# Performance work log

Measured on AMD Instinct MI355X. Metric: run time of the kernel, lower is better.

## Reference

```python
import jax, jax.numpy as jnp
import numpy as np

VOCAB, D = 10000, 32
QUEUE_LEN = 100


def setup_inputs() -> dict:
    key = jax.random.key(0)
    ks = jax.random.split(key, 8)
    B, T = 64, 1024
    s = 0.1
    return dict(
        inputs=jax.random.randint(ks[0], (B, T), 0, 10000, dtype=jnp.int32),
        emb=jax.random.normal(ks[1], (VOCAB, D), dtype=jnp.float32) * s,
        k_lstm=jax.random.normal(ks[2], (D, 4 * D), dtype=jnp.float32) * s,
        rk_lstm=jax.random.normal(ks[3], (D, 4 * D), dtype=jnp.float32) * s,
        b_lstm=jnp.zeros((4 * D,), dtype=jnp.float32),
        W1=jax.random.normal(ks[4], (D, D), dtype=jnp.float32) * s,
        b1=jnp.zeros((D,), dtype=jnp.float32),
        W2=jax.random.normal(ks[5], (D, 1), dtype=jnp.float32) * s,
        b2=jnp.zeros((1,), dtype=jnp.float32),
    )


def _lstm(x, k, rk, b):
    # Keras LSTM, gate order [i, f, g(cell), o], sigmoid recurrent act, tanh act.
    B, T, D = x.shape
    xg = jnp.einsum('btd,de->bte', x, k) + b  # precompute input projections

    def step(carry, xg_t):
        h, c = carry
        z = xg_t + h @ rk
        i, f, g, o = jnp.split(z, 4, axis=-1)
        c = jax.nn.sigmoid(f) * c + jax.nn.sigmoid(i) * jnp.tanh(g)
        h = jax.nn.sigmoid(o) * jnp.tanh(c)
        return (h, c), h

    init = (jnp.zeros((B, D), x.dtype), jnp.zeros((B, D), x.dtype))
    _, hs = jax.lax.scan(step, init, jnp.swapaxes(xg, 0, 1))  # [T,B,D]
    return jnp.swapaxes(hs, 0, 1)  # [B,T,D]


def _zero_index_queue(x_ids):
    # Vectorized replacement of the (i,j) Python scan: last QUEUE_LEN positions
    # (row-major order) where token==0, as [QUEUE_LEN,2] int32, padded with -1.
    B, T = x_ids.shape
    flat = (x_ids == 0).reshape(-1)
    N = flat.shape[0]
    ridx = jnp.nonzero(flat[::-1], size=QUEUE_LEN, fill_value=-1)[0]
    pos = jnp.where(ridx >= 0, N - 1 - ridx, -1)[::-1]  # ascending, like deque
    ii = jnp.where(pos >= 0, pos // T, -1)
    jj = jnp.where(pos >= 0, pos % T, -1)
    return jnp.stack([ii, jj], axis=-1).astype(jnp.int32)


def _forward_float(x_ids, emb, k_lstm, rk_lstm, b_lstm, W1, b1, W2, b2):
    x = emb[x_ids]                                  # [B,T,D]
    h = _lstm(x, k_lstm, rk_lstm, b_lstm)           # [B,T,D]
    scores = jnp.einsum('btd,bsd->bts', h, h)       # unscaled dot attention
    attn = jax.nn.softmax(scores, axis=-1)
    ctx = jnp.einsum('bts,bsd->btd', attn, h)       # Keras Attention output
    y = jnp.einsum('btd,bte->bde', ctx, h)          # Dot(axes=(1,1)) -> [B,D,D]
    y = jax.nn.relu(y @ W1 + b1)
    return jax.nn.sigmoid(y @ W2 + b2)              # [B,D,1]


def reference(inputs, emb, k_lstm, rk_lstm, b_lstm, W1, b1, W2, b2):
    x_ids = jnp.where(inputs < VOCAB, inputs, 0)
    out = _forward_float(x_ids, emb, k_lstm, rk_lstm, b_lstm, W1, b1, W2, b2)
    return out, _zero_index_queue(x_ids)
```

## Files before the change

### kernel.cpp

```cpp
#include <hip/hip_runtime.h>
#include <math.h>

#define BB 64
#define TT 1024
#define DD 32
#define GG 128
#define VOCABN 10000
#define QLEN 100

typedef short short8 __attribute__((ext_vector_type(8)));
typedef float floatx4 __attribute__((ext_vector_type(4)));
typedef float floatx2 __attribute__((ext_vector_type(2)));
typedef unsigned short u16;

__device__ __forceinline__ float fsig(float x) {
    return __builtin_amdgcn_rcpf(1.0f + __expf(-x));
}
__device__ __forceinline__ float readlane_f(float v, int l) {
    return __int_as_float(__builtin_amdgcn_readlane(__float_as_int(v), l));
}
__device__ __forceinline__ u16 f2bf_rne(float x) {
    unsigned u = __float_as_uint(x);
    u += 0x7FFF + ((u >> 16) & 1);
    return (u16)(u >> 16);
}
__device__ __forceinline__ float bf2f(u16 s) {
    return __uint_as_float(((unsigned)s) << 16);
}
__device__ __forceinline__ floatx2 fma2(float s, floatx2 w, floatx2 acc) {
    return __builtin_elementwise_fma((floatx2){s, s}, w, acc);
}

#define UU 8
__global__
__attribute__((amdgpu_flat_work_group_size(128, 128)))
__attribute__((amdgpu_waves_per_eu(1, 1)))
void k_lstm_scan(const int* __restrict__ ids,
                 const float* __restrict__ emb,
                 const float* __restrict__ klstm,
                 const float* __restrict__ bias,
                 const float* __restrict__ rk,
                 u16* __restrict__ hh, u16* __restrict__ hl,
                 u16* __restrict__ th, u16* __restrict__ tl,
                 int* __restrict__ list,
                 float* __restrict__ outq) {
    const int b = blockIdx.x;
    const int tid = threadIdx.x;
    const int wv = tid >> 6;
    const int l = tid & 63;
    if (b >= BB) {
        if (wv != 0) return;
        const int4* v4 = (const int4*)ids;
        const int C4 = (BB * TT) / 4 / 64;
        const int b4 = l * C4;
        int cnt = 0;
#pragma unroll 4
        for (int i = 0; i < C4; ++i) {
            int4 v = v4[b4 + i];
            cnt += (v.x == 0 || (unsigned)v.x >= VOCABN);
            cnt += (v.y == 0 || (unsigned)v.y >= VOCABN);
            cnt += (v.z == 0 || (unsigned)v.z >= VOCABN);
            cnt += (v.w == 0 || (unsigned)v.w >= VOCABN);
        }
        int scan = cnt;
#pragma unroll
        for (int o = 1; o < 64; o <<= 1) {
            int nn = __shfl_up(scan, o);
            if (l >= o) scan += nn;
        }
        const int total = __shfl(scan, 63);
        int off = scan - cnt;
        const int base = l * (C4 * 4);
#pragma unroll 4
        for (int i = 0; i < C4; ++i) {
            int4 v = v4[b4 + i];
            if (v.x == 0 || (unsigned)v.x >= VOCABN) list[off++] = base + 4 * i;
            if (v.y == 0 || (unsigned)v.y >= VOCABN) list[off++] = base + 4 * i + 1;
            if (v.z == 0 || (unsigned)v.z >= VOCABN) list[off++] = base + 4 * i + 2;
            if (v.w == 0 || (unsigned)v.w >= VOCABN) list[off++] = base + 4 * i + 3;
        }
        __threadfence();
        const int Kc = total < QLEN ? total : QLEN;
        for (int t = l; t < QLEN; t += 64) {
            float ii = -1.0f, jj = -1.0f;
            if (t >= QLEN - Kc) {
                int pos = list[total - QLEN + t];
                ii = (float)(pos >> 10);
                jj = (float)(pos & (TT - 1));
            }
            outq[2 * t] = ii;
            outq[2 * t + 1] = jj;
        }
        return;
    }

    __shared__ float ring[2][UU][GG];
    __shared__ __align__(16) float hring[2][UU][DD];
    const int* idsb = ids + b * TT;

    if (wv == 1) {
        const int ja = l, jb = l + 64;
        floatx2 kp[DD];
#pragma unroll
        for (int d2 = 0; d2 < DD; ++d2)
            kp[d2] = (floatx2){klstm[d2 * GG + ja], klstm[d2 * GG + jb]};
        const floatx2 bj = (floatx2){bias[ja], bias[jb]};
        const int dd = l & 31;
        const int u_r = l >> 3, dc = (l & 7) * 4;
        const int d_c = l & 31, ug = (l >> 5) * 4;
        u16* hhb = hh + (size_t)b * TT * DD;
        u16* hlb = hl + (size_t)b * TT * DD;
        u16* thb = th + (size_t)b * DD * TT;
        u16* tlb = tl + (size_t)b * DD * TT;

#define PROD_TOKEN(SEL, U, EV)                                               \
        {                                                                    \
            floatx2 z0 = bj;                                                 \
            floatx2 z1 = {0.f, 0.f}, z2 = {0.f, 0.f}, z3 = {0.f, 0.f};       \
            _Pragma("unroll")                                                \
            for (int k = 0; k < DD; k += 4) {                                \
                float e0 = readlane_f(EV, k);                                \
                float e1 = readlane_f(EV, k + 1);                            \
                float e2 = readlane_f(EV, k + 2);                            \
                float e3 = readlane_f(EV, k + 3);                            \
                z0 = fma2(e0, kp[k], z0);                                    \
                z1 = fma2(e1, kp[k + 1], z1);                                \
                z2 = fma2(e2, kp[k + 2], z2);                                \
                z3 = fma2(e3, kp[k + 3], z3);                                \
            }                                                                \
            floatx2 zf = (z0 + z1) + (z2 + z3);                              \
            ring[SEL][U][ja] = zf.x;                                         \
            ring[SEL][U][jb] = zf.y;                                         \
        }

#define CVT_CHUNK(HSEL, TC0)                                                 \
        {                                                                    \
            const float4 hv4 = *(const float4*)&hring[HSEL][u_r][dc];        \
            float xr[4] = {hv4.x, hv4.y, hv4.z, hv4.w};                      \
            u16 rh[4], rl[4];                                                \
            _Pragma("unroll")                                                \
            for (int i = 0; i < 4; ++i) {                                    \
                rh[i] = f2bf_rne(xr[i]);                                     \
                rl[i] = f2bf_rne(xr[i] - bf2f(rh[i]));                       \
            }                                                                \
            ushort4 rhv = {rh[0], rh[1], rh[2], rh[3]};                      \
            ushort4 rlv = {rl[0], rl[1], rl[2], rl[3]};                      \
            *(ushort4*)&hhb[(size_t)((TC0) + u_r) * DD + dc] = rhv;          \
            *(ushort4*)&hlb[(size_t)((TC0) + u_r) * DD + dc] = rlv;          \
            u16 ch[4], cl[4];                                                \
            _Pragma("unroll")                                                \
            for (int j = 0; j < 4; ++j) {                                    \
                float x = hring[HSEL][ug + j][d_c];                          \
                ch[j] = f2bf_rne(x);                                         \
                cl[j] = f2bf_rne(x - bf2f(ch[j]));                           \
            }                                                                \
            ushort4 chv = {ch[0], ch[1], ch[2], ch[3]};                      \
            ushort4 clv = {cl[0], cl[1], cl[2], cl[3]};                      \
            *(ushort4*)&thb[(size_t)d_c * TT + (TC0) + ug] = chv;            \
            *(ushort4*)&tlb[(size_t)d_c * TT + (TC0) + ug] = clv;            \
        }

        {
            int id0 = idsb[0]; if ((unsigned)id0 >= VOCABN) id0 = 0;
            float ec = emb[id0 * DD + dd];
#pragma unroll
            for (int u = 0; u < UU; ++u) {
                float en = 0.f;
                if (u + 1 < UU) {
                    int idn = idsb[u + 1]; if ((unsigned)idn >= VOCABN) idn = 0;
                    en = emb[idn * DD + dd];
                }
                PROD_TOKEN(0, u, ec)
                ec = en;
            }
        }
        __syncthreads();
        int sel = 0;
        for (int t0 = 0; t0 < TT; t0 += UU) {
            if (t0 + UU < TT) {
                const int s = sel ^ 1;
                int id0 = idsb[t0 + UU]; if ((unsigned)id0 >= VOCABN) id0 = 0;
                float ec = emb[id0 * DD + dd];
#pragma unroll
                for (int u = 0; u < UU; ++u) {
                    float en = 0.f;
                    if (u + 1 < UU) {
                        int tn = t0 + UU + u + 1;
                        if (tn > TT - 1) tn = TT - 1;
                        int idn = idsb[tn]; if ((unsigned)idn >= VOCABN) idn = 0;
                        en = emb[idn * DD + dd];
                    }
                    PROD_TOKEN(s, u, ec)
                    ec = en;
                }
            }
            if (t0) CVT_CHUNK((t0 / UU - 1) & 1, t0 - UU)
            __syncthreads();
            sel ^= 1;
        }
        CVT_CHUNK(1, TT - UU)
#undef PROD_TOKEN
#undef CVT_CHUNK
        return;
    }

    const int d = l & 31;
    const bool hi = l >= 32;
    const int ga = (hi ? 32 : 0) + d;
    const int gb = (hi ? 96 : 64) + d;
    floatx2 rkp[DD];
#pragma unroll
    for (int k = 0; k < DD; ++k)
        rkp[k] = (floatx2){rk[k * GG + ga], rk[k * GG + gb]};

    float h = 0.0f, c = 0.0f;
    __syncthreads();
    int sel = 0;
    for (int t0 = 0; t0 < TT; t0 += UU) {
        float pa[UU], pb[UU];
#pragma unroll
        for (int u = 0; u < UU; ++u) {
            pa[u] = ring[sel][u][ga];
            pb[u] = ring[sel][u][gb];
        }
#pragma unroll
        for (int u = 0; u < UU; ++u) {
            floatx2 x0 = {pa[u], pb[u]};
            floatx2 x1 = {0.f, 0.f}, x2 = {0.f, 0.f}, x3 = {0.f, 0.f};
#pragma unroll
            for (int k = 0; k < DD; k += 4) {
                float h0 = readlane_f(h, k);
                float h1 = readlane_f(h, k + 1);
                float h2 = readlane_f(h, k + 2);
                float h3 = readlane_f(h, k + 3);
                x0 = fma2(h0, rkp[k],     x0);
                x1 = fma2(h1, rkp[k + 1], x1);
                x2 = fma2(h2, rkp[k + 2], x2);
                x3 = fma2(h3, rkp[k + 3], x3);
            }
            floatx2 zf = (x0 + x1) + (x2 + x3);
            float za = zf.x, zb = zf.y;
            float a = fsig(za);
            float zbm = hi ? zb : 2.0f * zb;
            float s2 = fsig(zbm);
            float bv = hi ? s2 : 2.0f * s2 - 1.0f;
            auto r1 = __builtin_amdgcn_permlane32_swap(
                __float_as_int(bv), __float_as_int(a), false, false);
            auto r2 = __builtin_amdgcn_permlane32_swap(
                __float_as_int(a), __float_as_int(bv), false, false);
            float fg = __int_as_float(r1[0]);
            float og = __int_as_float(r2[0]);
            c = fmaf(fg, c, a * bv);
            float tc = 2.0f * fsig(2.0f * c) - 1.0f;
            h = og * tc;
            if (!hi) hring[sel][u][d] = h;
        }
        __syncthreads();
        sel ^= 1;
    }
}

__global__ __launch_bounds__(256, 1) void k_attn(const u16* __restrict__ hh,
                                                 const u16* __restrict__ hl,
                                                 const u16* __restrict__ th,
                                                 const u16* __restrict__ tl,
                                                 u16* __restrict__ cth,
                                                 u16* __restrict__ ctl) {
    __shared__ __align__(16) char smem[4][20480];
    const int tid = threadIdx.x;
    const int w = tid >> 6;
    const int l = tid & 63;
    const int m = l & 15;
    const int g = l >> 4;
    const int b = blockIdx.x & 63;
    const int qt = (blockIdx.x >> 6) * 4 + w;
    const int q0 = qt * 64;
    const size_t rb = (size_t)b * TT * DD;
    const size_t tb = (size_t)b * DD * TT;
    u16* plw = (u16*)smem[w];

    const short8 Qh0 = *(const short8*)&hh[rb + (size_t)(q0 + m) * DD + g * 8];
    const short8 Ql0 = *(const short8*)&hl[rb + (size_t)(q0 + m) * DD + g * 8];
    const short8 Qh1 = *(const short8*)&hh[rb + (size_t)(q0 + 16 + m) * DD + g * 8];
    const short8 Ql1 = *(const short8*)&hl[rb + (size_t)(q0 + 16 + m) * DD + g * 8];
    const short8 Qh2 = *(const short8*)&hh[rb + (size_t)(q0 + 32 + m) * DD + g * 8];
    const short8 Ql2 = *(const short8*)&hl[rb + (size_t)(q0 + 32 + m) * DD + g * 8];
    const short8 Qh3 = *(const short8*)&hh[rb + (size_t)(q0 + 48 + m) * DD + g * 8];
    const short8 Ql3 = *(const short8*)&hl[rb + (size_t)(q0 + 48 + m) * DD + g * 8];
    short8 ONES;
#pragma unroll
    for (int j = 0; j < 8; ++j) ONES[j] = (short)0x3F80;

    floatx4 c0 = {0.f, 0.f, 0.f, 0.f}, c1 = {0.f, 0.f, 0.f, 0.f};
    floatx4 c2 = {0.f, 0.f, 0.f, 0.f}, c3 = {0.f, 0.f, 0.f, 0.f};
    floatx4 c4 = {0.f, 0.f, 0.f, 0.f}, c5 = {0.f, 0.f, 0.f, 0.f};
    floatx4 c6 = {0.f, 0.f, 0.f, 0.f}, c7 = {0.f, 0.f, 0.f, 0.f};
    floatx4 la0 = {0.f, 0.f, 0.f, 0.f}, la1 = {0.f, 0.f, 0.f, 0.f};
    floatx4 la2 = {0.f, 0.f, 0.f, 0.f}, la3 = {0.f, 0.f, 0.f, 0.f};

#define S_BLOCK(QH, QL, KH_A, KL_A, KH_B, KL_B, SA, SB)                       \
    SA = __builtin_amdgcn_mfma_f32_16x16x32_bf16(QH, KH_A, SA, 0, 0, 0);      \
    SA = __builtin_amdgcn_mfma_f32_16x16x32_bf16(QH, KL_A, SA, 0, 0, 0);      \
    SA = __builtin_amdgcn_mfma_f32_16x16x32_bf16(QL, KH_A, SA, 0, 0, 0);      \
    SB = __builtin_amdgcn_mfma_f32_16x16x32_bf16(QH, KH_B, SB, 0, 0, 0);      \
    SB = __builtin_amdgcn_mfma_f32_16x16x32_bf16(QH, KL_B, SB, 0, 0, 0);      \
    SB = __builtin_amdgcn_mfma_f32_16x16x32_bf16(QL, KH_B, SB, 0, 0, 0);

#define EXP_STORE(SA, SB, TILE, SLOT, PN)                                     \
    {                                                                         \
        u16* lp = plw + (((TILE) * 2 + (SLOT)) * 2 + (PN)) * 640;             \
        _Pragma("unroll")                                                     \
        for (int r = 0; r < 4; ++r) {                                         \
            lp[(g * 4 + r) * 40 + m]      = f2bf_rne(__expf(SA[r]));          \
            lp[(g * 4 + r) * 40 + 16 + m] = f2bf_rne(__expf(SB[r]));          \
        }                                                                     \
    }

#define SPANEL(KhA, KlA, KhB, KlB, SLOT, PN)                                  \
    {                                                                         \
        floatx4 sA = {0.f, 0.f, 0.f, 0.f}, sB = {0.f, 0.f, 0.f, 0.f};         \
        floatx4 tA = {0.f, 0.f, 0.f, 0.f}, tB = {0.f, 0.f, 0.f, 0.f};         \
        floatx4 uA = {0.f, 0.f, 0.f, 0.f}, uB = {0.f, 0.f, 0.f, 0.f};         \
        floatx4 vA = {0.f, 0.f, 0.f, 0.f}, vB = {0.f, 0.f, 0.f, 0.f};         \
        S_BLOCK(Qh0, Ql0, KhA, KlA, KhB, KlB, sA, sB)                         \
        S_BLOCK(Qh1, Ql1, KhA, KlA, KhB, KlB, tA, tB)                         \
        S_BLOCK(Qh2, Ql2, KhA, KlA, KhB, KlB, uA, uB)                         \
        S_BLOCK(Qh3, Ql3, KhA, KlA, KhB, KlB, vA, vB)                         \
        EXP_STORE(sA, sB, 0, SLOT, PN)                                        \
        EXP_STORE(tA, tB, 1, SLOT, PN)                                        \
        EXP_STORE(uA, uB, 2, SLOT, PN)                                        \
        EXP_STORE(vA, vB, 3, SLOT, PN)                                        \
    }

#define PV_TILE(T, CA, CB, LAc, SLOTP, PN, VH0, VL0, VH1, VL1)                \
    {                                                                         \
        const short8 P = *(const short8*)&plw[(((T) * 2 + (SLOTP)) * 2 + (PN)) * 640 + m * 40 + g * 8]; \
        CA  = __builtin_amdgcn_mfma_f32_16x16x32_bf16(P, VH0, CA, 0, 0, 0);   \
        CA  = __builtin_amdgcn_mfma_f32_16x16x32_bf16(P, VL0, CA, 0, 0, 0);   \
        CB  = __builtin_amdgcn_mfma_f32_16x16x32_bf16(P, VH1, CB, 0, 0, 0);   \
        CB  = __builtin_amdgcn_mfma_f32_16x16x32_bf16(P, VL1, CB, 0, 0, 0);   \
        LAc = __builtin_amdgcn_mfma_f32_16x16x32_bf16(P, ONES, LAc, 0, 0, 0); \
    }

#define PV_PANEL(SLOTP, PN, VH0, VL0, VH1, VL1)                               \
    PV_TILE(0, c0, c1, la0, SLOTP, PN, VH0, VL0, VH1, VL1)                    \
    PV_TILE(1, c2, c3, la1, SLOTP, PN, VH0, VL0, VH1, VL1)                    \
    PV_TILE(2, c4, c5, la2, SLOTP, PN, VH0, VL0, VH1, VL1)                    \
    PV_TILE(3, c6, c7, la3, SLOTP, PN, VH0, VL0, VH1, VL1)

#define LOAD_K(BASE, RA, RLA, RB, RLB)                                        \
    RA  = *(const short8*)&hh[rb + (size_t)((BASE) + m) * DD + g * 8];        \
    RLA = *(const short8*)&hl[rb + (size_t)((BASE) + m) * DD + g * 8];        \
    RB  = *(const short8*)&hh[rb + (size_t)((BASE) + 16 + m) * DD + g * 8];   \
    RLB = *(const short8*)&hl[rb + (size_t)((BASE) + 16 + m) * DD + g * 8];

#define LOAD_V(BASE, RH0, RL0, RH1, RL1)                                      \
    RH0 = *(const short8*)&th[tb + (size_t)m * TT + (BASE) + g * 8];          \
    RL0 = *(const short8*)&tl[tb + (size_t)m * TT + (BASE) + g * 8];          \
    RH1 = *(const short8*)&th[tb + (size_t)(16 + m) * TT + (BASE) + g * 8];   \
    RL1 = *(const short8*)&tl[tb + (size_t)(16 + m) * TT + (BASE) + g * 8];

    {
        short8 KA, KLA, KB, KLB;
        LOAD_K(0, KA, KLA, KB, KLB)
        SPANEL(KA, KLA, KB, KLB, 0, 0)
        LOAD_K(32, KA, KLA, KB, KLB)
        SPANEL(KA, KLA, KB, KLB, 0, 1)
    }
    short8 V0h0, V0l0, V0h1, V0l1, V1h0, V1l0, V1h1, V1l1;
    short8 K0hA, K0lA, K0hB, K0lB, K1hA, K1lA, K1hB, K1lB;
    LOAD_V(0,  V0h0, V0l0, V0h1, V0l1)
    LOAD_V(32, V1h0, V1l0, V1h1, V1l1)
    LOAD_K(64, K0hA, K0lA, K0hB, K0lB)
    LOAD_K(96, K1hA, K1lA, K1hB, K1lB)

#pragma unroll 1
    for (int j = 1; j < 16; ++j) {
        const int kb = (j < 15) ? 64 * (j + 1) : 0;
        const int vb = 64 * j;
        short8 nK0hA, nK0lA, nK0hB, nK0lB, nK1hA, nK1lA, nK1hB, nK1lB;
        short8 nV0h0, nV0l0, nV0h1, nV0l1, nV1h0, nV1l0, nV1h1, nV1l1;
        LOAD_K(kb,      nK0hA, nK0lA, nK0hB, nK0lB)
        LOAD_K(kb + 32, nK1hA, nK1lA, nK1hB, nK1lB)
        LOAD_V(vb,      nV0h0, nV0l0, nV0h1, nV0l1)
        LOAD_V(vb + 32, nV1h0, nV1l0, nV1h1, nV1l1)

        const int sl = j & 1;
        SPANEL(K0hA, K0lA, K0hB, K0lB, sl, 0)
        SPANEL(K1hA, K1lA, K1hB, K1lB, sl, 1)

        const int sp = (j - 1) & 1;
        PV_PANEL(sp, 0, V0h0, V0l0, V0h1, V0l1)
        PV_PANEL(sp, 1, V1h0, V1l0, V1h1, V1l1)

        K0hA = nK0hA; K0lA = nK0lA; K0hB = nK0hB; K0lB = nK0lB;
        K1hA = nK1hA; K1lA = nK1lA; K1hB = nK1hB; K1lB = nK1lB;
        V0h0 = nV0h0; V0l0 = nV0l0; V0h1 = nV0h1; V0l1 = nV0l1;
        V1h0 = nV1h0; V1l0 = nV1l0; V1h1 = nV1h1; V1l1 = nV1l1;
    }
    PV_PANEL(1, 0, V0h0, V0l0, V0h1, V0l1)
    PV_PANEL(1, 1, V1h0, V1l0, V1h1, V1l1)
#undef S_BLOCK
#undef EXP_STORE
#undef SPANEL
#undef PV_TILE
#undef PV_PANEL
#undef LOAD_K
#undef LOAD_V

    float (*ct)[34] = (float (*)[34])smem[w];
#pragma unroll
    for (int r = 0; r < 4; ++r) {
        float li0 = __builtin_amdgcn_rcpf(la0[r]);
        float li1 = __builtin_amdgcn_rcpf(la1[r]);
        float li2 = __builtin_amdgcn_rcpf(la2[r]);
        float li3 = __builtin_amdgcn_rcpf(la3[r]);
        ct[g * 4 + r][m]            = c0[r] * li0;
        ct[g * 4 + r][16 + m]       = c1[r] * li0;
        ct[16 + g * 4 + r][m]       = c2[r] * li1;
        ct[16 + g * 4 + r][16 + m]  = c3[r] * li1;
        ct[32 + g * 4 + r][m]       = c4[r] * li2;
        ct[32 + g * 4 + r][16 + m]  = c5[r] * li2;
        ct[48 + g * 4 + r][m]       = c6[r] * li3;
        ct[48 + g * 4 + r][16 + m]  = c7[r] * li3;
    }
    const int srow = l >> 3;
    const int tcol = (l & 7) * 8;
#pragma unroll
    for (int cblk = 0; cblk < 4; ++cblk) {
        const int dr = cblk * 8 + srow;
        short8 hvec, lvec;
#pragma unroll
        for (int j2 = 0; j2 < 8; ++j2) {
            float v = ct[tcol + j2][dr];
            u16 hv = f2bf_rne(v);
            hvec[j2] = (short)hv;
            lvec[j2] = (short)f2bf_rne(v - bf2f(hv));
        }
        *(short8*)&cth[tb + (size_t)dr * TT + q0 + tcol] = hvec;
        *(short8*)&ctl[tb + (size_t)dr * TT + q0 + tcol] = lvec;
    }
}

__global__ __launch_bounds__(256) void k_ymlp(const u16* __restrict__ cth,
                                              const u16* __restrict__ ctl,
                                              const u16* __restrict__ th,
                                              const u16* __restrict__ tl,
                                              const float* __restrict__ W1,
                                              const float* __restrict__ b1,
                                              const float* __restrict__ W2,
                                              const float* __restrict__ b2,
                                              float* __restrict__ out) {
    const int b = blockIdx.x;
    const int tid = threadIdx.x;
    const int w = tid >> 6;
    const int l = tid & 63;
    const int m = l & 15;
    const int g = l >> 4;
    const size_t tb = (size_t)b * DD * TT;
    const int k0 = w * (TT / 4);

    floatx4 y00 = {0.f, 0.f, 0.f, 0.f}, y01 = {0.f, 0.f, 0.f, 0.f};
    floatx4 y10 = {0.f, 0.f, 0.f, 0.f}, y11 = {0.f, 0.f, 0.f, 0.f};
#pragma unroll 2
    for (int ks = 0; ks < TT / 4; ks += 32) {
        const size_t kk = (size_t)(k0 + ks + g * 8);
        short8 A0h = *(const short8*)&cth[tb + (size_t)m * TT + kk];
        short8 A0l = *(const short8*)&ctl[tb + (size_t)m * TT + kk];
        short8 A1h = *(const short8*)&cth[tb + (size_t)(16 + m) * TT + kk];
        short8 A1l = *(const short8*)&ctl[tb + (size_t)(16 + m) * TT + kk];
        short8 B0h = *(const short8*)&th[tb + (size_t)m * TT + kk];
        short8 B0l = *(const short8*)&tl[tb + (size_t)m * TT + kk];
        short8 B1h = *(const short8*)&th[tb + (size_t)(16 + m) * TT + kk];
        short8 B1l = *(const short8*)&tl[tb + (size_t)(16 + m) * TT + kk];
        y00 = __builtin_amdgcn_mfma_f32_16x16x32_bf16(A0h, B0h, y00, 0, 0, 0);
        y00 = __builtin_amdgcn_mfma_f32_16x16x32_bf16(A0h, B0l, y00, 0, 0, 0);
        y00 = __builtin_amdgcn_mfma_f32_16x16x32_bf16(A0l, B0h, y00, 0, 0, 0);
        y01 = __builtin_amdgcn_mfma_f32_16x16x32_bf16(A0h, B1h, y01, 0, 0, 0);
        y01 = __builtin_amdgcn_mfma_f32_16x16x32_bf16(A0h, B1l, y01, 0, 0, 0);
        y01 = __builtin_amdgcn_mfma_f32_16x16x32_bf16(A0l, B1h, y01, 0, 0, 0);
        y10 = __builtin_amdgcn_mfma_f32_16x16x32_bf16(A1h, B0h, y10, 0, 0, 0);
        y10 = __builtin_amdgcn_mfma_f32_16x16x32_bf16(A1h, B0l, y10, 0, 0, 0);
        y10 = __builtin_amdgcn_mfma_f32_16x16x32_bf16(A1l, B0h, y10, 0, 0, 0);
        y11 = __builtin_amdgcn_mfma_f32_16x16x32_bf16(A1h, B1h, y11, 0, 0, 0);
        y11 = __builtin_amdgcn_mfma_f32_16x16x32_bf16(A1h, B1l, y11, 0, 0, 0);
        y11 = __builtin_amdgcn_mfma_f32_16x16x32_bf16(A1l, B1h, y11, 0, 0, 0);
    }
    __shared__ float ysp[4][DD][DD];
#pragma unroll
    for (int r = 0; r < 4; ++r) {
        ysp[w][g * 4 + r][m]           = y00[r];
        ysp[w][g * 4 + r][16 + m]      = y01[r];
        ysp[w][16 + g * 4 + r][m]      = y10[r];
        ysp[w][16 + g * 4 + r][16 + m] = y11[r];
    }
    __syncthreads();
    const int e = tid & 31;
    const int d4 = (tid >> 5) * 4;
    __shared__ float ys[DD][DD];
#pragma unroll
    for (int r = 0; r < 4; ++r)
        ys[d4 + r][e] = (ysp[0][d4 + r][e] + ysp[1][d4 + r][e])
                      + (ysp[2][d4 + r][e] + ysp[3][d4 + r][e]);
    __syncthreads();
    __shared__ float yr[DD][33];
#pragma unroll
    for (int r = 0; r < 4; ++r) {
        float v = b1[e];
#pragma unroll
        for (int ee = 0; ee < DD; ++ee) v += ys[d4 + r][ee] * W1[ee * DD + e];
        yr[d4 + r][e] = fmaxf(v, 0.0f);
    }
    __syncthreads();
    if (tid < DD) {
        float v = b2[0];
#pragma unroll
        for (int ee = 0; ee < DD; ++ee) v += yr[tid][ee] * W2[ee];
        out[b * DD + tid] = 1.0f / (1.0f + expf(-v));
    }
}

extern "C" void kernel_launch(void* const* d_in, const int* in_sizes, int n_in,
                              void* d_out, int out_size, void* d_ws, size_t ws_size,
                              hipStream_t stream) {
    const int* ids   = (const int*)d_in[0];
    const float* emb = (const float*)d_in[1];
    const float* kl  = (const float*)d_in[2];
    const float* rk  = (const float*)d_in[3];
    const float* bl  = (const float*)d_in[4];
    const float* W1  = (const float*)d_in[5];
    const float* b1  = (const float*)d_in[6];
    const float* W2  = (const float*)d_in[7];
    const float* b2  = (const float*)d_in[8];
    float* out = (float*)d_out;

    char* ws = (char*)d_ws;
    const size_t H_ELEMS = (size_t)BB * TT * DD;
    u16* hh   = (u16*)ws;
    u16* hl   = (u16*)(ws + H_ELEMS * 2);
    u16* th   = (u16*)(ws + H_ELEMS * 4);
    u16* tl   = (u16*)(ws + H_ELEMS * 6);
    u16* cth  = (u16*)(ws + H_ELEMS * 8 + H_ELEMS * 4);
    u16* ctl  = (u16*)(ws + H_ELEMS * 8 + H_ELEMS * 4 + H_ELEMS * 2);
    int* list = (int*)(ws + H_ELEMS * 8 + H_ELEMS * 8);

    k_lstm_scan<<<BB + 1, 128, 0, stream>>>(ids, emb, kl, bl, rk,
                                            hh, hl, th, tl, list, out + BB * DD);
    k_attn<<<BB * 4, 256, 0, stream>>>(hh, hl, th, tl, cth, ctl);
    k_ymlp<<<BB, 256, 0, stream>>>(cth, ctl, th, tl, W1, b1, W2, b2, out);
}
```

Measured before the change: 358.9 us.

## Split attention key range across two wave groups and reduce partial accumulators via LDS

Doubles the attention block to 512 threads, so each query tile is processed by two waves that each cover half of the key/value sequence. Their partial context and row-sum accumulators are combined through shared memory before normalisation. This is meant to raise wave-level parallelism and latency hiding in the attention stage, since only 256 blocks cover the GPU. In exchange it adds extra shared-memory traffic, two block barriers and a larger LDS footprint, and the pipelined inner loop now handles narrower 32-key panels.

```diff
diff --git a/kernel.cpp b/kernel.cpp
--- a/kernel.cpp
+++ b/kernel.cpp
@@ -260,24 +260,27 @@
     }
 }
 
-__global__ __launch_bounds__(256, 1) void k_attn(const u16* __restrict__ hh,
+__global__ __launch_bounds__(512, 1) void k_attn(const u16* __restrict__ hh,
                                                  const u16* __restrict__ hl,
                                                  const u16* __restrict__ th,
                                                  const u16* __restrict__ tl,
                                                  u16* __restrict__ cth,
                                                  u16* __restrict__ ctl) {
-    __shared__ __align__(16) char smem[4][20480];
+    __shared__ __align__(16) char smem[88064];
     const int tid = threadIdx.x;
     const int w = tid >> 6;
+    const int wt = w & 3;
+    const int kh = w >> 2;
     const int l = tid & 63;
     const int m = l & 15;
     const int g = l >> 4;
     const int b = blockIdx.x & 63;
-    const int qt = (blockIdx.x >> 6) * 4 + w;
+    const int qt = (blockIdx.x >> 6) * 4 + wt;
     const int q0 = qt * 64;
+    const int e0 = kh * 512;
     const size_t rb = (size_t)b * TT * DD;
     const size_t tb = (size_t)b * DD * TT;
-    u16* plw = (u16*)smem[w];
+    u16* plw = (u16*)(smem + w * 10240);
 
     const short8 Qh0 = *(const short8*)&hh[rb + (size_t)(q0 + m) * DD + g * 8];
     const short8 Ql0 = *(const short8*)&hl[rb + (size_t)(q0 + m) * DD + g * 8];
@@ -306,9 +309,9 @@
     SB = __builtin_amdgcn_mfma_f32_16x16x32_bf16(QH, KL_B, SB, 0, 0, 0);      \
     SB = __builtin_amdgcn_mfma_f32_16x16x32_bf16(QL, KH_B, SB, 0, 0, 0);
 
-#define EXP_STORE(SA, SB, TILE, SLOT, PN)                                     \
+#define EXP_STORE(SA, SB, TILE, SLOT)                                         \
     {                                                                         \
-        u16* lp = plw + (((TILE) * 2 + (SLOT)) * 2 + (PN)) * 640;             \
+        u16* lp = plw + ((TILE) * 2 + (SLOT)) * 640;                          \
         _Pragma("unroll")                                                     \
         for (int r = 0; r < 4; ++r) {                                         \
             lp[(g * 4 + r) * 40 + m]      = f2bf_rne(__expf(SA[r]));          \
@@ -316,7 +319,7 @@
         }                                                                     \
     }
 
-#define SPANEL(KhA, KlA, KhB, KlB, SLOT, PN)                                  \
+#define SPANEL(KhA, KlA, KhB, KlB, SLOT)                                      \
     {                                                                         \
         floatx4 sA = {0.f, 0.f, 0.f, 0.f}, sB = {0.f, 0.f, 0.f, 0.f};         \
         floatx4 tA = {0.f, 0.f, 0.f, 0.f}, tB = {0.f, 0.f, 0.f, 0.f};         \
@@ -326,15 +329,15 @@
         S_BLOCK(Qh1, Ql1, KhA, KlA, KhB, KlB, tA, tB)                         \
         S_BLOCK(Qh2, Ql2, KhA, KlA, KhB, KlB, uA, uB)                         \
         S_BLOCK(Qh3, Ql3, KhA, KlA, KhB, KlB, vA, vB)                         \
-        EXP_STORE(sA, sB, 0, SLOT, PN)                                        \
-        EXP_STORE(tA, tB, 1, SLOT, PN)                                        \
-        EXP_STORE(uA, uB, 2, SLOT, PN)                                        \
-        EXP_STORE(vA, vB, 3, SLOT, PN)                                        \
-    }
-
-#define PV_TILE(T, CA, CB, LAc, SLOTP, PN, VH0, VL0, VH1, VL1)                \
+        EXP_STORE(sA, sB, 0, SLOT)                                            \
+        EXP_STORE(tA, tB, 1, SLOT)                                            \
+        EXP_STORE(uA, uB, 2, SLOT)                                            \
+        EXP_STORE(vA, vB, 3, SLOT)                                            \
+    }
+
+#define PV_TILE(T, CA, CB, LAc, SLOTP, VH0, VL0, VH1, VL1)                    \
     {                                                                         \
-        const short8 P = *(const short8*)&plw[(((T) * 2 + (SLOTP)) * 2 + (PN)) * 640 + m * 40 + g * 8]; \
+        const short8 P = *(const short8*)&plw[((T) * 2 + (SLOTP)) * 640 + m * 40 + g * 8]; \
         CA  = __builtin_amdgcn_mfma_f32_16x16x32_bf16(P, VH0, CA, 0, 0, 0);   \
         CA  = __builtin_amdgcn_mfma_f32_16x16x32_bf16(P, VL0, CA, 0, 0, 0);   \
         CB  = __builtin_amdgcn_mfma_f32_16x16x32_bf16(P, VH1, CB, 0, 0, 0);   \
@@ -342,11 +345,11 @@
         LAc = __builtin_amdgcn_mfma_f32_16x16x32_bf16(P, ONES, LAc, 0, 0, 0); \
     }
 
-#define PV_PANEL(SLOTP, PN, VH0, VL0, VH1, VL1)                               \
-    PV_TILE(0, c0, c1, la0, SLOTP, PN, VH0, VL0, VH1, VL1)                    \
-    PV_TILE(1, c2, c3, la1, SLOTP, PN, VH0, VL0, VH1, VL1)                    \
-    PV_TILE(2, c4, c5, la2, SLOTP, PN, VH0, VL0, VH1, VL1)                    \
-    PV_TILE(3, c6, c7, la3, SLOTP, PN, VH0, VL0, VH1, VL1)
+#define PV_PANEL(SLOTP, VH0, VL0, VH1, VL1)                                   \
+    PV_TILE(0, c0, c1, la0, SLOTP, VH0, VL0, VH1, VL1)                        \
+    PV_TILE(1, c2, c3, la1, SLOTP, VH0, VL0, VH1, VL1)                        \
+    PV_TILE(2, c4, c5, la2, SLOTP, VH0, VL0, VH1, VL1)                        \
+    PV_TILE(3, c6, c7, la3, SLOTP, VH0, VL0, VH1, VL1)
 
 #define LOAD_K(BASE, RA, RLA, RB, RLB)                                        \
     RA  = *(const short8*)&hh[rb + (size_t)((BASE) + m) * DD + g * 8];        \
@@ -362,44 +365,28 @@
 
     {
         short8 KA, KLA, KB, KLB;
-        LOAD_K(0, KA, KLA, KB, KLB)
-        SPANEL(KA, KLA, KB, KLB, 0, 0)
-        LOAD_K(32, KA, KLA, KB, KLB)
-        SPANEL(KA, KLA, KB, KLB, 0, 1)
-    }
-    short8 V0h0, V0l0, V0h1, V0l1, V1h0, V1l0, V1h1, V1l1;
-    short8 K0hA, K0lA, K0hB, K0lB, K1hA, K1lA, K1hB, K1lB;
-    LOAD_V(0,  V0h0, V0l0, V0h1, V0l1)
-    LOAD_V(32, V1h0, V1l0, V1h1, V1l1)
-    LOAD_K(64, K0hA, K0lA, K0hB, K0lB)
-    LOAD_K(96, K1hA, K1lA, K1hB, K1lB)
+        LOAD_K(e0, KA, KLA, KB, KLB)
+        SPANEL(KA, KLA, KB, KLB, 0)
+    }
+    short8 Vh0, Vl0, Vh1, Vl1, KhA, KlA, KhB, KlB;
+    LOAD_V(e0, Vh0, Vl0, Vh1, Vl1)
+    LOAD_K(e0 + 32, KhA, KlA, KhB, KlB)
 
 #pragma unroll 1
     for (int j = 1; j < 16; ++j) {
-        const int kb = (j < 15) ? 64 * (j + 1) : 0;
-        const int vb = 64 * j;
-        short8 nK0hA, nK0lA, nK0hB, nK0lB, nK1hA, nK1lA, nK1hB, nK1lB;
-        short8 nV0h0, nV0l0, nV0h1, nV0l1, nV1h0, nV1l0, nV1h1, nV1l1;
-        LOAD_K(kb,      nK0hA, nK0lA, nK0hB, nK0lB)
-        LOAD_K(kb + 32, nK1hA, nK1lA, nK1hB, nK1lB)
-        LOAD_V(vb,      nV0h0, nV0l0, nV0h1, nV0l1)
-        LOAD_V(vb + 32, nV1h0, nV1l0, nV1h1, nV1l1)
-
-        const int sl = j & 1;
-        SPANEL(K0hA, K0lA, K0hB, K0lB, sl, 0)
-        SPANEL(K1hA, K1lA, K1hB, K1lB, sl, 1)
-
-        const int sp = (j - 1) & 1;
-        PV_PANEL(sp, 0, V0h0, V0l0, V0h1, V0l1)
-        PV_PANEL(sp, 1, V1h0, V1l0, V1h1, V1l1)
-
-        K0hA = nK0hA; K0lA = nK0lA; K0hB = nK0hB; K0lB = nK0lB;
-        K1hA = nK1hA; K1lA = nK1lA; K1hB = nK1hB; K1lB = nK1lB;
-        V0h0 = nV0h0; V0l0 = nV0l0; V0h1 = nV0h1; V0l1 = nV0l1;
-        V1h0 = nV1h0; V1l0 = nV1l0; V1h1 = nV1h1; V1l1 = nV1l1;
-    }
-    PV_PANEL(1, 0, V0h0, V0l0, V0h1, V0l1)
-    PV_PANEL(1, 1, V1h0, V1l0, V1h1, V1l1)
+        const int knK = (j < 15) ? e0 + 32 * (j + 1) : 0;
+        const int knV = e0 + 32 * j;
+        short8 nKhA, nKlA, nKhB, nKlB, nVh0, nVl0, nVh1, nVl1;
+        LOAD_K(knK, nKhA, nKlA, nKhB, nKlB)
+        LOAD_V(knV, nVh0, nVl0, nVh1, nVl1)
+
+        SPANEL(KhA, KlA, KhB, KlB, j & 1)
+        PV_PANEL((j - 1) & 1, Vh0, Vl0, Vh1, Vl1)
+
+        KhA = nKhA; KlA = nKlA; KhB = nKhB; KlB = nKlB;
+        Vh0 = nVh0; Vl0 = nVl0; Vh1 = nVh1; Vl1 = nVl1;
+    }
+    PV_PANEL(1, Vh0, Vl0, Vh1, Vl1)
 #undef S_BLOCK
 #undef EXP_STORE
 #undef SPANEL
@@ -408,7 +395,23 @@
 #undef LOAD_K
 #undef LOAD_V
 
-    float (*ct)[34] = (float (*)[34])smem[w];
+    __syncthreads();
+    if (w >= 4) {
+        floatx4* dst = (floatx4*)(smem + wt * 13312 + l * 208);
+        dst[0] = c0;  dst[1] = c1;  dst[2] = c2;  dst[3] = c3;
+        dst[4] = c4;  dst[5] = c5;  dst[6] = c6;  dst[7] = c7;
+        dst[8] = la0; dst[9] = la1; dst[10] = la2; dst[11] = la3;
+    }
+    __syncthreads();
+    if (w >= 4) return;
+    {
+        const floatx4* src = (const floatx4*)(smem + wt * 13312 + l * 208);
+        c0 += src[0];  c1 += src[1];  c2 += src[2];  c3 += src[3];
+        c4 += src[4];  c5 += src[5];  c6 += src[6];  c7 += src[7];
+        la0 += src[8]; la1 += src[9]; la2 += src[10]; la3 += src[11];
+    }
+
+    float (*ct)[34] = (float (*)[34])(smem + 53248 + w * 8704);
 #pragma unroll
     for (int r = 0; r < 4; ++r) {
         float li0 = __builtin_amdgcn_rcpf(la0[r]);
@@ -546,6 +549,6 @@
 
     k_lstm_scan<<<BB + 1, 128, 0, stream>>>(ids, emb, kl, bl, rk,
                                             hh, hl, th, tl, list, out + BB * DD);
-    k_attn<<<BB * 4, 256, 0, stream>>>(hh, hl, th, tl, cth, ctl);
+    k_attn<<<BB * 4, 512, 0, stream>>>(hh, hl, th, tl, cth, ctl);
     k_ymlp<<<BB, 256, 0, stream>>>(cth, ctl, th, tl, W1, b1, W2, b2, out);
 }
```

New measurement: 348.5 us. 2.9% less time.
